# Performance work log

Measured on AMD Instinct MI355X. Metric: run time of the kernel, lower is better.

The kernel has to match this reference:

```python
import jax, jax.numpy as jnp
import numpy as np

H = 1024      # hidden_dim
NH = 16       # num_heads
HD = H // NH  # head_dim
FF = 4 * H
EPS = 1e-5

def _ln(x, g, b):
    m = jnp.mean(x, axis=-1, keepdims=True)
    v = jnp.var(x, axis=-1, keepdims=True)
    return (x - m) * jax.lax.rsqrt(v + EPS) * g + b

def setup_inputs() -> dict:
    key = jax.random.key(0)
    ks = jax.random.split(key, 12)
    s = 1.0 / np.sqrt(H)
    inp = {
        'x': jax.random.normal(ks[0], (2, 2048, H), dtype=jnp.float32),
        'Wq': jax.random.normal(ks[1], (H, H), dtype=jnp.float32) * s,
        'bq': jnp.zeros((H,), dtype=jnp.float32),
        'Wk': jax.random.normal(ks[2], (H, H), dtype=jnp.float32) * s,
        'bk': jnp.zeros((H,), dtype=jnp.float32),
        'Wv': jax.random.normal(ks[3], (H, H), dtype=jnp.float32) * s,
        'bv': jnp.zeros((H,), dtype=jnp.float32),
        'Wo': jax.random.normal(ks[4], (H, H), dtype=jnp.float32) * s,
        'bo': jnp.zeros((H,), dtype=jnp.float32),
        'g1': jnp.ones((H,), dtype=jnp.float32),
        'b1': jnp.zeros((H,), dtype=jnp.float32),
        'W1': jax.random.normal(ks[5], (H, FF), dtype=jnp.float32) * s,
        'bf1': jnp.zeros((FF,), dtype=jnp.float32),
        'W2': jax.random.normal(ks[6], (FF, H), dtype=jnp.float32) * (1.0 / np.sqrt(FF)),
        'bf2': jnp.zeros((H,), dtype=jnp.float32),
        'g2': jnp.ones((H,), dtype=jnp.float32),
        'b2': jnp.zeros((H,), dtype=jnp.float32),
    }
    return inp

def reference(x, Wq, bq, Wk, bk, Wv, bv, Wo, bo, g1, b1, W1, bf1, W2, bf2, g2, b2):
    B, S, _ = x.shape
    residual = x
    xn = _ln(x, g1, b1)
    # [B,S,H] -> [B,NH,S,HD]
    def split_heads(t):
        return t.reshape(B, S, NH, HD).transpose(0, 2, 1, 3)
    q = split_heads(xn @ Wq + bq)
    k = split_heads(xn @ Wk + bk)
    v = split_heads(xn @ Wv + bv)
    scores = jnp.einsum('bhqd,bhkd->bhqk', q, k) / np.sqrt(HD).astype(np.float32)
    attn = jax.nn.softmax(scores, axis=-1)
    ctx = jnp.einsum('bhqk,bhkd->bhqd', attn, v)
    ctx = ctx.transpose(0, 2, 1, 3).reshape(B, S, H)
    out = ctx @ Wo + bo + residual
    residual = out
    on = _ln(out, g2, b2)
    out = jax.nn.relu(on @ W1 + bf1) @ W2 + bf2 + residual
    return out
```

## Files before the change

### kernel.cpp

```cpp
#include <hip/hip_runtime.h>
#include <hip/hip_bf16.h>

constexpr int HDIM = 1024;
constexpr int NHEAD = 16;
constexpr int FFDIM = 4096;
constexpr int SEQLEN = 2048;
constexpr int NTOK = 4096;

typedef __bf16 bf16x8 __attribute__((ext_vector_type(8)));
typedef float f32x4 __attribute__((ext_vector_type(4)));
typedef short s16x4 __attribute__((ext_vector_type(4)));

union U16x8 {
    s16x4 h[2];
    bf16x8 v;
    int4 raw;
    short s[8];
};

__device__ __forceinline__ short f2bf(float f) {
    union { float f; unsigned u; } c;
    c.f = f;
    return (short)((c.u + 0x8000u) >> 16);
}

__device__ __forceinline__ void gload16(const void* gsrc, void* lds) {
    __builtin_amdgcn_global_load_lds(
        (const __attribute__((address_space(1))) unsigned int*)gsrc,
        (__attribute__((address_space(3))) unsigned int*)lds, 16, 0, 0);
}


constexpr float QSCALE = 0.18033688011112042f;

__global__ __launch_bounds__(256)
void wconv_all(const float* __restrict__ Wq, const float* __restrict__ Wk,
               const float* __restrict__ Wv, const float* __restrict__ Wo,
               const float* __restrict__ W1, const float* __restrict__ W2,
               short* __restrict__ qkvT, short* __restrict__ WoT,
               short* __restrict__ W1T, short* __restrict__ W2T) {
    int i = blockIdx.x;
    const float* W;
    short* WT;
    int K, N, bx, by;
    if (i < 2048) {
        const int w = i >> 9;
        i &= 511;
        K = HDIM; N = HDIM; bx = i & 3; by = i >> 2;
        W = w == 0 ? Wq : w == 1 ? Wk : w == 2 ? Wv : Wo;
        WT = w == 3 ? WoT : qkvT + (size_t)w * HDIM * HDIM;
    } else if (i < 4096) {
        i -= 2048;
        K = HDIM; N = FFDIM; bx = i & 15; by = i >> 4;
        W = W1; WT = W1T;
    } else {
        i -= 4096;
        K = FFDIM; N = HDIM; bx = i & 3; by = i >> 2;
        W = W2; WT = W2T;
    }
    const int n = bx * 256 + threadIdx.x;
    const int g = by >> 2, fc = by & 3;
    const int k0 = g * 32 + fc * 4;
    s16x4 lo, hi;
#pragma unroll
    for (int j = 0; j < 4; ++j) lo[j] = f2bf(W[(size_t)(k0 + j) * N + n]);
#pragma unroll
    for (int j = 0; j < 4; ++j) hi[j] = f2bf(W[(size_t)(k0 + 16 + j) * N + n]);
    short* dst = WT + (size_t)n * K + by * 8;
    *(s16x4*)dst = lo;
    *(s16x4*)(dst + 4) = hi;
}

__global__ __launch_bounds__(256)
void ln_bf16(const float* __restrict__ x, const float* __restrict__ g,
             const float* __restrict__ b, short* __restrict__ out) {
    const int row = blockIdx.x, t = threadIdx.x;
    const float* xr = x + (size_t)row * HDIM;
    float4 v = *(const float4*)&xr[t * 4];
    float s = v.x + v.y + v.z + v.w;
    float ss = v.x * v.x + v.y * v.y + v.z * v.z + v.w * v.w;
#pragma unroll
    for (int o = 32; o > 0; o >>= 1) {
        s += __shfl_down(s, o);
        ss += __shfl_down(ss, o);
    }
    __shared__ float red[8];
    const int wv = t >> 6, ln = t & 63;
    if (ln == 0) { red[wv] = s; red[4 + wv] = ss; }
    __syncthreads();
    s = red[0] + red[1] + red[2] + red[3];
    ss = red[4] + red[5] + red[6] + red[7];
    const float mean = s * (1.0f / HDIM);
    const float var = ss * (1.0f / HDIM) - mean * mean;
    const float rstd = rsqrtf(var + 1e-5f);
    float4 gv = *(const float4*)&g[t * 4];
    float4 bv = *(const float4*)&b[t * 4];
    s16x4 o4;
    o4[0] = f2bf((v.x - mean) * rstd * gv.x + bv.x);
    o4[1] = f2bf((v.y - mean) * rstd * gv.y + bv.y);
    o4[2] = f2bf((v.z - mean) * rstd * gv.z + bv.z);
    o4[3] = f2bf((v.w - mean) * rstd * gv.w + bv.w);
    const int kk = (t * 4) & 31;
    const int dst = ((t * 4) & ~31) + ((kk & 15) >> 2) * 8 + (kk >> 4) * 4;
    *(s16x4*)&out[(size_t)row * HDIM + dst] = o4;
}

template <int BM, int BN, int MODE>
__global__ __launch_bounds__(256, 3)
void gemm_bf16(const short* __restrict__ A, const short* __restrict__ BT,
               const float* __restrict__ bias, const float* __restrict__ resid,
               void* __restrict__ outp, int M, int N, int K,
               const float* __restrict__ bias2, const float* __restrict__ bias3,
               void* __restrict__ out3) {
    constexpr int MI = BM / 32, NJ = BN / 32;
    constexpr int NSEG = (BM + BN) / 16;
    __shared__ short LdsF[2 * (BM + BN) * 32];
    const int tid = threadIdx.x;
    const int lane = tid & 63, wave = tid >> 6;
    const int wm = wave >> 1, wn = wave & 1;
    const int l15 = lane & 15, lg = lane >> 4;
    const int lsw = lg ^ ((l15 >> 1) & 3);
    const int m0 = blockIdx.x * BM, n0 = blockIdx.y * BN;
    const int nk = K >> 5;
    const int sr = lane >> 2;
    const int sc8 = (((lane & 3) ^ ((sr >> 1) & 3))) * 8;

    auto stage = [&](int buf, int kt) {
#pragma unroll
        for (int p = 0; p < NSEG / 4; ++p) {
            const int s = wave + p * 4;
            const short* src = (s < BM / 16)
                ? A + (size_t)(m0 + s * 16 + sr) * K + kt * 32 + sc8
                : BT + (size_t)(n0 + (s - BM / 16) * 16 + sr) * K + kt * 32 + sc8;
            const int off = __builtin_amdgcn_readfirstlane(buf * (BM + BN) * 64 + s * 1024);
            gload16(src, (char*)LdsF + off);
        }
    };

    f32x4 acc[MI][NJ] = {};
    stage(0, 0);
    for (int kt = 0; kt < nk; ++kt) {
        const int buf = kt & 1;
        __syncthreads();
        if (kt + 1 < nk) stage(buf ^ 1, kt + 1);
        bf16x8 af[MI], bfr[NJ];
#pragma unroll
        for (int i = 0; i < MI; ++i)
            af[i] = *(const bf16x8*)&LdsF[buf * (BM + BN) * 32 +
                                          (wm * (BM / 2) + i * 16 + l15) * 32 + lsw * 8];
#pragma unroll
        for (int j = 0; j < NJ; ++j)
            bfr[j] = *(const bf16x8*)&LdsF[buf * (BM + BN) * 32 +
                                           (BM + wn * (BN / 2) + j * 16 + l15) * 32 + lsw * 8];
#pragma unroll
        for (int i = 0; i < MI; ++i)
#pragma unroll
            for (int j = 0; j < NJ; ++j)
                acc[i][j] = __builtin_amdgcn_mfma_f32_16x16x32_bf16(af[i], bfr[j], acc[i][j], 0, 0, 0);
    }

    const int rbase = m0 + wm * (BM / 2);
    const int cbase = n0 + wn * (BN / 2);
    if constexpr (MODE == 0) {
#pragma unroll
        for (int i = 0; i < MI; ++i)
#pragma unroll
            for (int j = 0; j < NJ; ++j) {
                const int c = cbase + j * 16 + l15;
                const float bv = bias[c];
#pragma unroll
                for (int ii = 0; ii < 4; ++ii) {
                    const int r = rbase + i * 16 + lg * 4 + ii;
                    const size_t idx = (size_t)r * N + c;
                    ((float*)outp)[idx] = acc[i][j][ii] + bv + resid[idx];
                }
            }
    } else if constexpr (MODE == 1) {
#pragma unroll
        for (int i = 0; i < MI; ++i)
#pragma unroll
            for (int j = 0; j < NJ; ++j) {
                const int c = cbase + j * 16 + l15;
                const float bv = bias[c];
                const int cp = (c & ~31) | ((l15 >> 2) * 8 + (j & 1) * 4 + (l15 & 3));
#pragma unroll
                for (int ii = 0; ii < 4; ++ii) {
                    const int r = rbase + i * 16 + lg * 4 + ii;
                    float v = acc[i][j][ii] + bv;
                    v = v > 0.0f ? v : 0.0f;
                    ((short*)outp)[(size_t)r * N + cp] = f2bf(v);
                }
            }
    } else {
        const int which = n0 >> 10;
        if (which < 2) {
            const float* bb = which == 0 ? bias : bias2;
            const float qs = which == 0 ? QSCALE : 1.0f;
            short* QKp = (short*)outp;
#pragma unroll
            for (int i = 0; i < MI; ++i)
#pragma unroll
                for (int j = 0; j < NJ; ++j) {
                    const int c = cbase + j * 16 + l15;
                    const float bv = bb[c & 1023];
                    const int cp = (c & ~31) | ((l15 >> 2) * 8 + (j & 1) * 4 + (l15 & 3));
#pragma unroll
                    for (int ii = 0; ii < 4; ++ii) {
                        const int r = rbase + i * 16 + lg * 4 + ii;
                        QKp[(size_t)r * 2048 + cp] = f2bf((acc[i][j][ii] + bv) * qs);
                    }
                }
        } else {
            short* VTp = (short*)out3;
#pragma unroll
            for (int j = 0; j < NJ; ++j) {
                const int c = cbase + j * 16 + l15;
                const int cc = c - 2048;
                const int hh = cc >> 6, dd = cc & 63;
                const float bv = bias3[cc];
#pragma unroll
                for (int i = 0; i < MI; ++i) {
                    const int r0 = rbase + i * 16 + lg * 4;
                    const int bb_ = r0 >> 11;
                    const int s0 = r0 & (SEQLEN - 1);
                    const int sbase = (s0 & ~31) + lg * 8 + (i & 1) * 4;
                    s16x4 v4;
#pragma unroll
                    for (int ii = 0; ii < 4; ++ii) v4[ii] = f2bf(acc[i][j][ii] + bv);
                    *(s16x4*)&VTp[(((size_t)(bb_ * NHEAD + hh)) * 64 + dd) * SEQLEN + sbase] = v4;
                }
            }
        }
    }
}

__global__ __launch_bounds__(256, 4)
void attn_fwd(const short* __restrict__ QK, const short* __restrict__ VT,
              short* __restrict__ ctx) {
    __shared__ short KlF[2 * 4096];
    __shared__ short VlF[2 * 4096];
    const int tid = threadIdx.x, lane = tid & 63, wave = tid >> 6;
    const int l15 = lane & 15, lg = lane >> 4;
    const int lsw = lg ^ ((l15 >> 1) & 3);
    const int qt = blockIdx.x, bh = blockIdx.y;
    const int b = bh >> 4, h = bh & 15;
    const size_t tokbase = (size_t)b * SEQLEN;
    const short* Kbase = QK + 1024 + h * 64;
    const short* Vbase = VT + (size_t)bh * 64 * SEQLEN;
    const int sr = lane >> 2;
    const int sc8 = (((lane & 3) ^ ((sr >> 1) & 3))) * 8;

    auto stage = [&](int buf, int kt) {
#pragma unroll
        for (int p = 0; p < 2; ++p) {
            const int seg = wave + p * 4;
            const int ks = seg >> 2, rb = (seg & 3) * 16;
            const int off = __builtin_amdgcn_readfirstlane(buf * 8192 + seg * 1024);
            gload16(Kbase + (tokbase + kt * 64 + rb + sr) * 2048 + ks * 32 + sc8,
                    (char*)KlF + off);
            gload16(Vbase + (size_t)(rb + sr) * SEQLEN + kt * 64 + ks * 32 + sc8,
                    (char*)VlF + off);
        }
    };

    const short* qp = QK + (tokbase + qt * 64 + wave * 16 + l15) * 2048 + h * 64;
    bf16x8 qf[2];
    qf[0] = *(const bf16x8*)(qp + lg * 8);
    qf[1] = *(const bf16x8*)(qp + 32 + lg * 8);

    U16x8 uo;
#pragma unroll
    for (int j = 0; j < 8; ++j) uo.s[j] = 0x3F80;
    const bf16x8 onesv = uo.v;

    f32x4 o[4] = {};
    f32x4 Lacc = {};
    float Mi = -INFINITY;
    stage(0, 0);
    for (int kt = 0; kt < SEQLEN / 64; ++kt) {
        const int buf = kt & 1;
        __syncthreads();
        if (kt + 1 < SEQLEN / 64) stage(buf ^ 1, kt + 1);

        f32x4 sc[4];
        __builtin_amdgcn_s_setprio(1);
#pragma unroll
        for (int j = 0; j < 4; ++j) {
            bf16x8 kf0 = *(const bf16x8*)&KlF[buf * 4096 + (j * 16 + l15) * 32 + lsw * 8];
            bf16x8 kf1 = *(const bf16x8*)&KlF[buf * 4096 + 2048 + (j * 16 + l15) * 32 + lsw * 8];
            f32x4 z = {};
            z = __builtin_amdgcn_mfma_f32_16x16x32_bf16(kf0, qf[0], z, 0, 0, 0);
            sc[j] = __builtin_amdgcn_mfma_f32_16x16x32_bf16(kf1, qf[1], z, 0, 0, 0);
        }
        __builtin_amdgcn_s_setprio(0);

        const float a0 = fmaxf(fmaxf(sc[0][0], sc[0][1]), sc[0][2]);
        const float a1 = fmaxf(fmaxf(sc[0][3], sc[1][0]), sc[1][1]);
        const float a2 = fmaxf(fmaxf(sc[1][2], sc[1][3]), sc[2][0]);
        const float a3 = fmaxf(fmaxf(sc[2][1], sc[2][2]), sc[2][3]);
        const float a4 = fmaxf(fmaxf(sc[3][0], sc[3][1]), sc[3][2]);
        const float b0 = fmaxf(fmaxf(a0, a1), sc[3][3]);
        const float b1 = fmaxf(fmaxf(a2, a3), a4);
        float pmax = fmaxf(b0, b1);
        pmax = fmaxf(pmax, __shfl_xor(pmax, 16));
        pmax = fmaxf(pmax, __shfl_xor(pmax, 32));
        if (__any(pmax > Mi + 8.0f)) {
            const float newM = fmaxf(Mi, pmax);
            const float fac = exp2f(Mi - newM);
            Lacc *= fac;
#pragma unroll
            for (int fd = 0; fd < 4; ++fd) o[fd] *= fac;
            Mi = newM;
        }
        U16x8 u0, u1;
#pragma unroll
        for (int ii = 0; ii < 4; ++ii) {
            u0.s[ii]     = f2bf(exp2f(sc[0][ii] - Mi));
            u0.s[4 + ii] = f2bf(exp2f(sc[1][ii] - Mi));
            u1.s[ii]     = f2bf(exp2f(sc[2][ii] - Mi));
            u1.s[4 + ii] = f2bf(exp2f(sc[3][ii] - Mi));
        }
        __builtin_amdgcn_s_setprio(1);
#pragma unroll
        for (int ks = 0; ks < 2; ++ks) {
            const bf16x8 pf = ks == 0 ? u0.v : u1.v;
            Lacc = __builtin_amdgcn_mfma_f32_16x16x32_bf16(onesv, pf, Lacc, 0, 0, 0);
#pragma unroll
            for (int fd = 0; fd < 4; ++fd) {
                bf16x8 vf = *(const bf16x8*)&VlF[buf * 4096 + ks * 2048 + (fd * 16 + l15) * 32 + lsw * 8];
                o[fd] = __builtin_amdgcn_mfma_f32_16x16x32_bf16(vf, pf, o[fd], 0, 0, 0);
            }
        }
        __builtin_amdgcn_s_setprio(0);
    }

    const float rl = 1.0f / Lacc[0];
    const int qrow = qt * 64 + wave * 16 + l15;
    short* crow = ctx + (tokbase + qrow) * HDIM + h * 64;
#pragma unroll
    for (int fd = 0; fd < 4; ++fd) {
        s16x4 v4;
#pragma unroll
        for (int ii = 0; ii < 4; ++ii) v4[ii] = f2bf(o[fd][ii] * rl);
        *(s16x4*)(crow + (fd >> 1) * 32 + lg * 8 + (fd & 1) * 4) = v4;
    }
}

extern "C" void kernel_launch(void* const* d_in, const int* in_sizes, int n_in,
                              void* d_out, int out_size, void* d_ws, size_t ws_size,
                              hipStream_t stream) {
    const float* x  = (const float*)d_in[0];
    const float* Wq = (const float*)d_in[1];
    const float* bq = (const float*)d_in[2];
    const float* Wk = (const float*)d_in[3];
    const float* bk = (const float*)d_in[4];
    const float* Wv = (const float*)d_in[5];
    const float* bv = (const float*)d_in[6];
    const float* Wo = (const float*)d_in[7];
    const float* bo = (const float*)d_in[8];
    const float* g1 = (const float*)d_in[9];
    const float* b1 = (const float*)d_in[10];
    const float* W1 = (const float*)d_in[11];
    const float* bf1 = (const float*)d_in[12];
    const float* W2 = (const float*)d_in[13];
    const float* bf2 = (const float*)d_in[14];
    const float* g2 = (const float*)d_in[15];
    const float* b2 = (const float*)d_in[16];

    char* ws = (char*)d_ws;
    const size_t MB = 1024 * 1024;
    short* qkvT = (short*)(ws + 0 * MB);
    short* WoT  = (short*)(ws + 6 * MB);
    short* W1T  = (short*)(ws + 8 * MB);
    short* W2T  = (short*)(ws + 16 * MB);
    short* xn   = (short*)(ws + 24 * MB);
    short* QKb  = (short*)(ws + 32 * MB);
    short* VTb  = (short*)(ws + 48 * MB);
    short* ctx  = (short*)(ws + 56 * MB);
    float* out1 = (float*)(ws + 64 * MB);
    short* h1   = (short*)(ws + 32 * MB);

    wconv_all<<<6144, 256, 0, stream>>>(Wq, Wk, Wv, Wo, W1, W2, qkvT, WoT, W1T, W2T);

    ln_bf16<<<NTOK, 256, 0, stream>>>(x, g1, b1, xn);

    gemm_bf16<128, 128, 2><<<dim3(NTOK / 128, 3072 / 128), 256, 0, stream>>>(
        xn, qkvT, bq, nullptr, QKb, NTOK, 3072, HDIM, bk, bv, VTb);

    attn_fwd<<<dim3(SEQLEN / 64, 32), 256, 0, stream>>>(QKb, VTb, ctx);

    gemm_bf16<128, 64, 0><<<dim3(NTOK / 128, HDIM / 64), 256, 0, stream>>>(
        ctx, WoT, bo, x, out1, NTOK, HDIM, HDIM, nullptr, nullptr, nullptr);

    ln_bf16<<<NTOK, 256, 0, stream>>>(out1, g2, b2, xn);

    gemm_bf16<128, 128, 1><<<dim3(NTOK / 128, FFDIM / 128), 256, 0, stream>>>(
        xn, W1T, bf1, nullptr, h1, NTOK, FFDIM, HDIM, nullptr, nullptr, nullptr);

    gemm_bf16<128, 64, 0><<<dim3(NTOK / 128, HDIM / 64), 256, 0, stream>>>(
        h1, W2T, bf2, out1, (float*)d_out, NTOK, HDIM, FFDIM, nullptr, nullptr, nullptr);
}
```

Baseline: 246.1 us.

## Use packed bf16 conversion, XCD-aware attention block mapping, simpler staging pointers

Replaces scalar float-to-bf16 rounding with packed hardware conversion in the weight conversion, layernorm, V-transpose epilogue and attention probability packing. Remaps the attention grid to a 1D launch in which consecutive blocks on the same XCD share a batch-head, aiming to improve L2 reuse of K/V. Simplifies K/V staging by using incrementing pointers, and defers the cross-lane max shuffle so it only runs when a rescale is needed. Conversion rounding changes from round-half-up to round-to-nearest-even, which slightly alters numerics.

```diff
diff --git a/kernel.cpp b/kernel.cpp
--- a/kernel.cpp
+++ b/kernel.cpp
@@ -15,6 +15,7 @@
     s16x4 h[2];
     bf16x8 v;
     int4 raw;
+    unsigned u[4];
     short s[8];
 };
 
@@ -22,6 +23,11 @@
     union { float f; unsigned u; } c;
     c.f = f;
     return (short)((c.u + 0x8000u) >> 16);
+}
+
+__device__ __forceinline__ unsigned cvtpk(float a, float b) {
+    __hip_bfloat162 h = __float22bfloat162_rn(float2{a, b});
+    return *reinterpret_cast<unsigned*>(&h);
 }
 
 __device__ __forceinline__ void gload16(const void* gsrc, void* lds) {
@@ -61,14 +67,17 @@
     const int n = bx * 256 + threadIdx.x;
     const int g = by >> 2, fc = by & 3;
     const int k0 = g * 32 + fc * 4;
-    s16x4 lo, hi;
-#pragma unroll
-    for (int j = 0; j < 4; ++j) lo[j] = f2bf(W[(size_t)(k0 + j) * N + n]);
-#pragma unroll
-    for (int j = 0; j < 4; ++j) hi[j] = f2bf(W[(size_t)(k0 + 16 + j) * N + n]);
-    short* dst = WT + (size_t)n * K + by * 8;
-    *(s16x4*)dst = lo;
-    *(s16x4*)(dst + 4) = hi;
+    float a[4], c[4];
+#pragma unroll
+    for (int j = 0; j < 4; ++j) a[j] = W[(size_t)(k0 + j) * N + n];
+#pragma unroll
+    for (int j = 0; j < 4; ++j) c[j] = W[(size_t)(k0 + 16 + j) * N + n];
+    U16x8 u;
+    u.u[0] = cvtpk(a[0], a[1]);
+    u.u[1] = cvtpk(a[2], a[3]);
+    u.u[2] = cvtpk(c[0], c[1]);
+    u.u[3] = cvtpk(c[2], c[3]);
+    *(int4*)(WT + (size_t)n * K + by * 8) = u.raw;
 }
 
 __global__ __launch_bounds__(256)
@@ -95,14 +104,12 @@
     const float rstd = rsqrtf(var + 1e-5f);
     float4 gv = *(const float4*)&g[t * 4];
     float4 bv = *(const float4*)&b[t * 4];
-    s16x4 o4;
-    o4[0] = f2bf((v.x - mean) * rstd * gv.x + bv.x);
-    o4[1] = f2bf((v.y - mean) * rstd * gv.y + bv.y);
-    o4[2] = f2bf((v.z - mean) * rstd * gv.z + bv.z);
-    o4[3] = f2bf((v.w - mean) * rstd * gv.w + bv.w);
+    union { s16x4 h4; uint2 u2; } pk;
+    pk.u2.x = cvtpk((v.x - mean) * rstd * gv.x + bv.x, (v.y - mean) * rstd * gv.y + bv.y);
+    pk.u2.y = cvtpk((v.z - mean) * rstd * gv.z + bv.z, (v.w - mean) * rstd * gv.w + bv.w);
     const int kk = (t * 4) & 31;
     const int dst = ((t * 4) & ~31) + ((kk & 15) >> 2) * 8 + (kk >> 4) * 4;
-    *(s16x4*)&out[(size_t)row * HDIM + dst] = o4;
+    *(s16x4*)&out[(size_t)row * HDIM + dst] = pk.h4;
 }
 
 template <int BM, int BN, int MODE>
@@ -224,10 +231,10 @@
                     const int bb_ = r0 >> 11;
                     const int s0 = r0 & (SEQLEN - 1);
                     const int sbase = (s0 & ~31) + lg * 8 + (i & 1) * 4;
-                    s16x4 v4;
-#pragma unroll
-                    for (int ii = 0; ii < 4; ++ii) v4[ii] = f2bf(acc[i][j][ii] + bv);
-                    *(s16x4*)&VTp[(((size_t)(bb_ * NHEAD + hh)) * 64 + dd) * SEQLEN + sbase] = v4;
+                    union { s16x4 h4; uint2 u2; } pk;
+                    pk.u2.x = cvtpk(acc[i][j][0] + bv, acc[i][j][1] + bv);
+                    pk.u2.y = cvtpk(acc[i][j][2] + bv, acc[i][j][3] + bv);
+                    *(s16x4*)&VTp[(((size_t)(bb_ * NHEAD + hh)) * 64 + dd) * SEQLEN + sbase] = pk.h4;
                 }
             }
         }
@@ -242,25 +249,24 @@
     const int tid = threadIdx.x, lane = tid & 63, wave = tid >> 6;
     const int l15 = lane & 15, lg = lane >> 4;
     const int lsw = lg ^ ((l15 >> 1) & 3);
-    const int qt = blockIdx.x, bh = blockIdx.y;
+    const int bid = blockIdx.x;
+    const int xcd = bid & 7, li = bid >> 3;
+    const int bh = xcd * 4 + (li >> 5);
+    const int qt = li & 31;
     const int b = bh >> 4, h = bh & 15;
     const size_t tokbase = (size_t)b * SEQLEN;
-    const short* Kbase = QK + 1024 + h * 64;
-    const short* Vbase = VT + (size_t)bh * 64 * SEQLEN;
     const int sr = lane >> 2;
     const int sc8 = (((lane & 3) ^ ((sr >> 1) & 3))) * 8;
 
-    auto stage = [&](int buf, int kt) {
-#pragma unroll
-        for (int p = 0; p < 2; ++p) {
-            const int seg = wave + p * 4;
-            const int ks = seg >> 2, rb = (seg & 3) * 16;
-            const int off = __builtin_amdgcn_readfirstlane(buf * 8192 + seg * 1024);
-            gload16(Kbase + (tokbase + kt * 64 + rb + sr) * 2048 + ks * 32 + sc8,
-                    (char*)KlF + off);
-            gload16(Vbase + (size_t)(rb + sr) * SEQLEN + kt * 64 + ks * 32 + sc8,
-                    (char*)VlF + off);
-        }
+    const short* kp = QK + (tokbase + wave * 16 + sr) * 2048 + 1024 + h * 64 + sc8;
+    const short* vp = VT + ((size_t)bh * 64 + wave * 16 + sr) * SEQLEN + sc8;
+
+    auto stage = [&](int buf) {
+        const int off = __builtin_amdgcn_readfirstlane(buf * 8192 + wave * 1024);
+        gload16(kp, (char*)KlF + off);
+        gload16(kp + 32, (char*)KlF + off + 4096);
+        gload16(vp, (char*)VlF + off);
+        gload16(vp + 32, (char*)VlF + off + 4096);
     };
 
     const short* qp = QK + (tokbase + qt * 64 + wave * 16 + l15) * 2048 + h * 64;
@@ -276,11 +282,15 @@
     f32x4 o[4] = {};
     f32x4 Lacc = {};
     float Mi = -INFINITY;
-    stage(0, 0);
+    stage(0);
     for (int kt = 0; kt < SEQLEN / 64; ++kt) {
         const int buf = kt & 1;
         __syncthreads();
-        if (kt + 1 < SEQLEN / 64) stage(buf ^ 1, kt + 1);
+        if (kt + 1 < SEQLEN / 64) {
+            kp += 64 * 2048;
+            vp += 64;
+            stage(buf ^ 1);
+        }
 
         f32x4 sc[4];
         __builtin_amdgcn_s_setprio(1);
@@ -300,26 +310,26 @@
         const float a3 = fmaxf(fmaxf(sc[2][1], sc[2][2]), sc[2][3]);
         const float a4 = fmaxf(fmaxf(sc[3][0], sc[3][1]), sc[3][2]);
         const float b0 = fmaxf(fmaxf(a0, a1), sc[3][3]);
-        const float b1 = fmaxf(fmaxf(a2, a3), a4);
-        float pmax = fmaxf(b0, b1);
-        pmax = fmaxf(pmax, __shfl_xor(pmax, 16));
-        pmax = fmaxf(pmax, __shfl_xor(pmax, 32));
-        if (__any(pmax > Mi + 8.0f)) {
-            const float newM = fmaxf(Mi, pmax);
-            const float fac = exp2f(Mi - newM);
+        const float lmax = fmaxf(b0, fmaxf(a2, fmaxf(a3, a4)));
+        if (__any(lmax > Mi + 8.0f)) {
+            float pmax = fmaxf(lmax, __shfl_xor(lmax, 16));
+            pmax = fmaxf(pmax, __shfl_xor(pmax, 32));
+            const float fac = exp2f(Mi - pmax);
             Lacc *= fac;
 #pragma unroll
             for (int fd = 0; fd < 4; ++fd) o[fd] *= fac;
-            Mi = newM;
+            Mi = pmax;
         }
         U16x8 u0, u1;
-#pragma unroll
-        for (int ii = 0; ii < 4; ++ii) {
-            u0.s[ii]     = f2bf(exp2f(sc[0][ii] - Mi));
-            u0.s[4 + ii] = f2bf(exp2f(sc[1][ii] - Mi));
-            u1.s[ii]     = f2bf(exp2f(sc[2][ii] - Mi));
-            u1.s[4 + ii] = f2bf(exp2f(sc[3][ii] - Mi));
-        }
+        u0.u[0] = cvtpk(exp2f(sc[0][0] - Mi), exp2f(sc[0][1] - Mi));
+        u0.u[1] = cvtpk(exp2f(sc[0][2] - Mi), exp2f(sc[0][3] - Mi));
+        u0.u[2] = cvtpk(exp2f(sc[1][0] - Mi), exp2f(sc[1][1] - Mi));
+        u0.u[3] = cvtpk(exp2f(sc[1][2] - Mi), exp2f(sc[1][3] - Mi));
+        u1.u[0] = cvtpk(exp2f(sc[2][0] - Mi), exp2f(sc[2][1] - Mi));
+        u1.u[1] = cvtpk(exp2f(sc[2][2] - Mi), exp2f(sc[2][3] - Mi));
+        u1.u[2] = cvtpk(exp2f(sc[3][0] - Mi), exp2f(sc[3][1] - Mi));
+        u1.u[3] = cvtpk(exp2f(sc[3][2] - Mi), exp2f(sc[3][3] - Mi));
+
         __builtin_amdgcn_s_setprio(1);
 #pragma unroll
         for (int ks = 0; ks < 2; ++ks) {
@@ -387,7 +397,7 @@
     gemm_bf16<128, 128, 2><<<dim3(NTOK / 128, 3072 / 128), 256, 0, stream>>>(
         xn, qkvT, bq, nullptr, QKb, NTOK, 3072, HDIM, bk, bv, VTb);
 
-    attn_fwd<<<dim3(SEQLEN / 64, 32), 256, 0, stream>>>(QKb, VTb, ctx);
+    attn_fwd<<<1024, 256, 0, stream>>>(QKb, VTb, ctx);
 
     gemm_bf16<128, 64, 0><<<dim3(NTOK / 128, HDIM / 64), 256, 0, stream>>>(
         ctx, WoT, bo, x, out1, NTOK, HDIM, HDIM, nullptr, nullptr, nullptr);
```

New measurement: 245.2 us. No clear change (-0.4%).
